# Kernel optimization log

Hardware: AMD Instinct MI355X
Metric: run time of the kernel (lower is better)

## Reference

```python
import jax, jax.numpy as jnp
import numpy as np

T, H, N = 4096, 2048, 1024  # seq_length, d_model, d_hidden
MAX_PHASE = 6.28


def setup_inputs() -> dict:
    key = jax.random.key(0)
    ks = jax.random.split(key, 9)
    inputs = jax.random.normal(ks[0], (T, H), dtype=jnp.float32)
    # LRU init (exp_param=True, r_min=0, r_max=1): lambda = exp(-exp(nu) + i*exp(theta))
    u1 = jax.random.uniform(ks[1], (N,), dtype=jnp.float32)
    u2 = jax.random.uniform(ks[2], (N,), dtype=jnp.float32)
    nu = jnp.log(-0.5 * jnp.log(u1))            # log-parameterized decay
    theta = jnp.log(MAX_PHASE * u2)             # log-parameterized phase
    # gamma_log = log(sqrt(1 - |lambda|^2)), |lambda| = exp(-exp(nu))
    gamma_log = 0.5 * jnp.log(1.0 - jnp.exp(-2.0 * jnp.exp(nu)) + 1e-8)
    B_re = jax.random.normal(ks[3], (N, H), dtype=jnp.float32) / np.sqrt(2 * H)
    B_im = jax.random.normal(ks[4], (N, H), dtype=jnp.float32) / np.sqrt(2 * H)
    C_re = jax.random.normal(ks[5], (H, N), dtype=jnp.float32) / np.sqrt(N)
    C_im = jax.random.normal(ks[6], (H, N), dtype=jnp.float32) / np.sqrt(N)
    D = jax.random.normal(ks[7], (H,), dtype=jnp.float32)
    return {"inputs": inputs, "nu": nu, "theta": theta, "gamma_log": gamma_log,
            "B_re": B_re, "B_im": B_im, "C_re": C_re, "C_im": C_im, "D": D}


def _binary_operator_diag(q_i, q_j):
    A_i, b_i = q_i
    A_j, b_j = q_j
    return (A_j * A_i, A_j * b_i + b_j)


def reference(inputs, nu, theta, gamma_log, B_re, B_im, C_re, C_im, D):
    # diag_lambda = exp(-exp(nu) + i*exp(theta))   (exp_param=True)
    diag_lambda = jnp.exp(-jnp.exp(nu) + 1j * jnp.exp(theta))      # [N] complex64
    gamma = jnp.exp(gamma_log)                                      # [N]
    B_norm = (B_re + 1j * B_im) * gamma[:, None]                    # [N, H] complex
    # Bu_t = B_norm @ u_t  ->  [T, N]
    Bu = inputs.astype(jnp.complex64) @ B_norm.T
    Lam = jnp.broadcast_to(diag_lambda[None, :], Bu.shape)          # [T, N]
    # parallel scan of diagonal linear recurrence h_t = lambda * h_{t-1} + Bu_t
    _, h = jax.lax.associative_scan(_binary_operator_diag, (Lam, Bu))
    C = C_re + 1j * C_im                                            # [H, N]
    # y_t = Re(C @ h_t) + D * u_t
    y = (h @ C.T).real + D[None, :] * inputs                        # [T, H]
    return y
```

## Files before the change

kernel.cpp:

```cpp
#include <hip/hip_runtime.h>
#include <math.h>

#define T_DIM 4096
#define H_DIM 2048
#define N_DIM 1024
#define N2    2048
#define KK    2048
#define CHUNK 64
#define NCHUNK (T_DIM / CHUNK)
#define NT    (KK / 64)

using u16    = unsigned short;
using u16x4  = __attribute__((ext_vector_type(4))) u16;
using bf16x8 = __attribute__((ext_vector_type(8))) short;
using f32x4  = __attribute__((ext_vector_type(4))) float;

typedef const __attribute__((address_space(1))) u16 glob_u16;
typedef __attribute__((address_space(3))) u16 lds_u16;

__device__ inline void gload16(const u16* g, u16* l) {
    __builtin_amdgcn_global_load_lds((glob_u16*)g, (lds_u16*)l, 16, 0, 0);
}

__device__ inline u16 f2bf(float x) {
    unsigned u = __builtin_bit_cast(unsigned, x);
    u += 0x7fffu + ((u >> 16) & 1u);
    return (u16)(u >> 16);
}
__device__ inline float bf2f(u16 x) {
    return __builtin_bit_cast(float, (unsigned)x << 16);
}

__global__ __launch_bounds__(256) void cvt_all_k(
    const float* __restrict__ U, const float* __restrict__ Bre,
    const float* __restrict__ Bim, const float* __restrict__ glog,
    const float* __restrict__ Cre, const float* __restrict__ Cim,
    u16* __restrict__ Ubf, u16* __restrict__ Bcat, u16* __restrict__ Ccat)
{
    int bid = blockIdx.x;
    if (bid < 8192) {
        size_t i = ((size_t)bid * 256 + threadIdx.x) * 4;
        float4 v = *(const float4*)(U + i);
        u16x4 o = { f2bf(v.x), f2bf(v.y), f2bf(v.z), f2bf(v.w) };
        *(u16x4*)(Ubf + i) = o;
    } else if (bid < 12288) {
        size_t i = ((size_t)(bid - 8192) * 256 + threadIdx.x) * 4;
        int n = (int)(i >> 11);
        size_t h = i & 2047;
        int nn = n & (N_DIM - 1);
        float g = expf(glog[nn]);
        const float* src = (n < N_DIM ? Bre : Bim) + (size_t)nn * H_DIM + h;
        float4 v = *(const float4*)src;
        u16x4 o = { f2bf(v.x * g), f2bf(v.y * g), f2bf(v.z * g), f2bf(v.w * g) };
        *(u16x4*)(Bcat + i) = o;
    } else {
        size_t i = ((size_t)(bid - 12288) * 256 + threadIdx.x) * 4;
        int hrow = (int)(i >> 11);
        int n = (int)(i & 2047);
        float sgn = 1.f;
        const float* src;
        if (n < N_DIM) src = Cre + (size_t)hrow * N_DIM + n;
        else { src = Cim + (size_t)hrow * N_DIM + (n - N_DIM); sgn = -1.f; }
        float4 v = *(const float4*)src;
        u16x4 o = { f2bf(v.x * sgn), f2bf(v.y * sgn), f2bf(v.z * sgn), f2bf(v.w * sgn) };
        *(u16x4*)(Ccat + i) = o;
    }
}

template <int EPI>
__global__ __launch_bounds__(512, 4) void gemm_pipe(
    const u16* __restrict__ A, const u16* __restrict__ B,
    void* __restrict__ Cout, const float* __restrict__ D,
    const u16* __restrict__ Ubf)
{
    __shared__ u16 lds[40960];

    const int tid  = threadIdx.x;
    const int wave = tid >> 6, lane = tid & 63;
    const int nbid = (blockIdx.x & 7) * 64 + (blockIdx.x >> 3);
    const int bm = nbid >> 4;
    const int bn = nbid & 15;
    const size_t row0 = (size_t)bm * 128;
    const size_t col0 = (size_t)bn * 128;
    const int kg = wave & 1;
    const int wc = (wave >> 1) & 1;
    const int wr = wave >> 2;
    const int fr = lane & 15, fq = lane >> 4;

    const int srow = wave * 16 + (lane >> 3);
    const int skc  = (lane & 7) ^ ((lane >> 3) & 7);
    const u16* aSrc = A + (row0 + srow) * KK + skc * 8;
    const u16* bSrc = B + (col0 + srow) * KK + skc * 8;
    const int stOff = wave * 1024;

    const int slot8 = ((kg * 4 + fq) ^ (fr & 7)) * 8;
    const int aOff = (wr * 64 + fr) * 64 + slot8;
    const int bOff = (wc * 64 + fr) * 64 + slot8;

    f32x4 acc[4][4] = {};

    auto STAGE_A = [&](int buf, int kt) {
        gload16(aSrc + kt * 64,            &lds[buf * 8192 + stOff]);
        gload16(aSrc + 8 * KK + kt * 64,   &lds[buf * 8192 + stOff + 512]);
    };
    auto STAGE_B = [&](int buf, int kt) {
        gload16(bSrc + kt * 64,            &lds[24576 + buf * 8192 + stOff]);
        gload16(bSrc + 8 * KK + kt * 64,   &lds[24576 + buf * 8192 + stOff + 512]);
    };

    bf16x8 fa[4], fb[4];
    auto READ_F = [&](const u16* Ab, const u16* Bb) {
#pragma unroll
        for (int m = 0; m < 4; ++m) fa[m] = *(const bf16x8*)&Ab[aOff + m * 1024];
#pragma unroll
        for (int n = 0; n < 4; ++n) fb[n] = *(const bf16x8*)&Bb[bOff + n * 1024];
    };

    STAGE_A(0, 0); STAGE_B(0, 0); STAGE_A(1, 1);
    asm volatile("s_waitcnt vmcnt(2)" ::: "memory");
    __builtin_amdgcn_s_barrier();
    READ_F(&lds[0], &lds[24576]);

    int a_cur = 0;
    for (int t = 0; t < NT; ++t) {
        if (t + 1 < NT) STAGE_B((t + 1) & 1, t + 1);
        __builtin_amdgcn_s_setprio(1);
#pragma unroll
        for (int m = 0; m < 4; ++m)
#pragma unroll
            for (int n = 0; n < 4; ++n)
                acc[m][n] = __builtin_amdgcn_mfma_f32_16x16x32_bf16(
                    fa[m], fb[n], acc[m][n], 0, 0, 0);
        __builtin_amdgcn_s_setprio(0);
        if (t + 2 < NT) {
            int a_nxt = a_cur + 2; if (a_nxt >= 3) a_nxt -= 3;
            STAGE_A(a_nxt, t + 2);
        }
        if (t + 1 < NT) {
            if (t + 2 < NT) asm volatile("s_waitcnt vmcnt(2)" ::: "memory");
            else            asm volatile("s_waitcnt vmcnt(0)" ::: "memory");
            __builtin_amdgcn_s_barrier();
            int a_n = a_cur + 1; if (a_n == 3) a_n = 0;
            READ_F(&lds[a_n * 8192], &lds[24576 + ((t + 1) & 1) * 8192]);
        }
        ++a_cur; if (a_cur == 3) a_cur = 0;
    }

    __builtin_amdgcn_s_barrier();
    const int pair = wr * 2 + wc;
    float* lf = (float*)lds;
    if (kg == 1) {
#pragma unroll
        for (int i = 0; i < 16; ++i)
            *(f32x4*)&lf[pair * 4096 + i * 256 + lane * 4] = acc[i >> 2][i & 3];
    }
    asm volatile("s_waitcnt lgkmcnt(0)" ::: "memory");
    __builtin_amdgcn_s_barrier();
    if (kg == 0) {
#pragma unroll
        for (int i = 0; i < 16; ++i) {
            f32x4 o = *(const f32x4*)&lf[pair * 4096 + i * 256 + lane * 4];
            acc[i >> 2][i & 3] += o;
        }
        const int crow = (int)row0 + wr * 64 + fq * 4;
        const int ccol = (int)col0 + wc * 64 + fr;
        float dc[4];
        if constexpr (EPI) {
#pragma unroll
            for (int n = 0; n < 4; ++n) dc[n] = D[ccol + n * 16];
        }
#pragma unroll
        for (int m = 0; m < 4; ++m)
#pragma unroll
            for (int n = 0; n < 4; ++n) {
                int cc = ccol + n * 16;
#pragma unroll
                for (int j = 0; j < 4; ++j) {
                    int r = crow + m * 16 + j;
                    size_t p = (size_t)r * N2 + cc;
                    float v = acc[m][n][j];
                    if constexpr (EPI)
                        ((float*)Cout)[p] = v + dc[n] * bf2f(Ubf[p]);
                    else
                        ((u16*)Cout)[p] = f2bf(v);
                }
            }
    }
}

__global__ __launch_bounds__(256) void carry_pass_k(const u16* __restrict__ Bu,
                                                    const float* __restrict__ nu,
                                                    const float* __restrict__ theta,
                                                    float* __restrict__ car) {
    int idx = blockIdx.x * 256 + threadIdx.x;
    int chan = idx & (N_DIM - 1);
    int chunk = idx >> 10;
    float a = expf(nu[chan]), b = expf(theta[chan]);
    float m = expf(-a), s, c;
    __sincosf(b, &s, &c);
    float lr = m * c, li = m * s;
    float hr = 0.f, hi = 0.f;
    size_t base = (size_t)chunk * CHUNK * N2 + chan;
    for (int i = 0; i < CHUNK; ++i) {
        size_t p = base + (size_t)i * N2;
        float br = bf2f(Bu[p]), bi = bf2f(Bu[p + N_DIM]);
        float nr = fmaf(lr, hr, fmaf(-li, hi, br));
        float ni = fmaf(lr, hi, fmaf(li, hr, bi));
        hr = nr; hi = ni;
    }
    car[(size_t)chunk * N2 + chan] = hr;
    car[(size_t)chunk * N2 + N_DIM + chan] = hi;
}

__global__ __launch_bounds__(256) void scan_carry_k(float* __restrict__ car,
                                                    const float* __restrict__ nu,
                                                    const float* __restrict__ theta) {
    __shared__ float sR[NCHUNK][65], sI[NCHUNK][65];
    int tid = threadIdx.x;
    int chan0 = blockIdx.x * 64;
    for (int i = tid; i < NCHUNK * 64; i += 256) {
        int ck = i >> 6, c = i & 63;
        sR[ck][c] = car[(size_t)ck * N2 + chan0 + c];
        sI[ck][c] = car[(size_t)ck * N2 + N_DIM + chan0 + c];
    }
    __syncthreads();
    if (tid < 64) {
        int chan = chan0 + tid;
        float a = expf(nu[chan]), b = expf(theta[chan]);
        float m = expf(-(float)CHUNK * a), s, c;
        __sincosf((float)CHUNK * b, &s, &c);
        float lr = m * c, li = m * s;
        float hr = sR[0][tid], hi = sI[0][tid];
        for (int ck = 1; ck < NCHUNK; ++ck) {
            float nr = fmaf(lr, hr, fmaf(-li, hi, sR[ck][tid]));
            float ni = fmaf(lr, hi, fmaf(li, hr, sI[ck][tid]));
            hr = nr; hi = ni;
            sR[ck][tid] = hr; sI[ck][tid] = hi;
        }
    }
    __syncthreads();
    for (int i = tid; i < NCHUNK * 64; i += 256) {
        int ck = i >> 6, c = i & 63;
        car[(size_t)ck * N2 + chan0 + c] = sR[ck][c];
        car[(size_t)ck * N2 + N_DIM + chan0 + c] = sI[ck][c];
    }
}

__global__ __launch_bounds__(256) void scan_out_k(const u16* __restrict__ Bu,
                                                  const float* __restrict__ car,
                                                  const float* __restrict__ nu,
                                                  const float* __restrict__ theta,
                                                  u16* __restrict__ Hbf) {
    int idx = blockIdx.x * 256 + threadIdx.x;
    int chan = idx & (N_DIM - 1);
    int chunk = idx >> 10;
    float a = expf(nu[chan]), b = expf(theta[chan]);
    float m = expf(-a), s, c;
    __sincosf(b, &s, &c);
    float lr = m * c, li = m * s;
    float hr = 0.f, hi = 0.f;
    if (chunk > 0) {
        size_t cp = (size_t)(chunk - 1) * N2 + chan;
        hr = car[cp]; hi = car[cp + N_DIM];
    }
    size_t base = (size_t)chunk * CHUNK * N2 + chan;
    for (int i = 0; i < CHUNK; ++i) {
        size_t p = base + (size_t)i * N2;
        float br = bf2f(Bu[p]), bi = bf2f(Bu[p + N_DIM]);
        float nr = fmaf(lr, hr, fmaf(-li, hi, br));
        float ni = fmaf(lr, hi, fmaf(li, hr, bi));
        hr = nr; hi = ni;
        Hbf[p] = f2bf(hr);
        Hbf[p + N_DIM] = f2bf(hi);
    }
}

extern "C" void kernel_launch(void* const* d_in, const int* in_sizes, int n_in,
                              void* d_out, int out_size, void* d_ws, size_t ws_size,
                              hipStream_t stream) {
    const float* U     = (const float*)d_in[0];
    const float* nu    = (const float*)d_in[1];
    const float* theta = (const float*)d_in[2];
    const float* glog  = (const float*)d_in[3];
    const float* Bre   = (const float*)d_in[4];
    const float* Bim   = (const float*)d_in[5];
    const float* Cre   = (const float*)d_in[6];
    const float* Cim   = (const float*)d_in[7];
    const float* Dp    = (const float*)d_in[8];
    float* Y = (float*)d_out;

    u16* Ubf  = (u16*)d_ws;
    u16* Bcat = Ubf + (size_t)T_DIM * H_DIM;
    u16* Ccat = Bcat + (size_t)N2 * H_DIM;
    u16* Hbf  = Ccat + (size_t)H_DIM * N2;
    u16* Bu   = Hbf + (size_t)T_DIM * N2;
    float* car = (float*)(Bu + (size_t)T_DIM * N2);

    cvt_all_k<<<16384, 256, 0, stream>>>(U, Bre, Bim, glog, Cre, Cim,
                                         Ubf, Bcat, Ccat);

    gemm_pipe<0><<<512, 512, 0, stream>>>(Ubf, Bcat, (void*)Bu, nullptr, nullptr);

    carry_pass_k<<<(NCHUNK * N_DIM) / 256, 256, 0, stream>>>(Bu, nu, theta, car);
    scan_carry_k<<<N_DIM / 64, 256, 0, stream>>>(car, nu, theta);
    scan_out_k<<<(NCHUNK * N_DIM) / 256, 256, 0, stream>>>(Bu, car, nu, theta, Hbf);

    gemm_pipe<1><<<512, 512, 0, stream>>>(Hbf, Ccat, (void*)Y, Dp, Ubf);
}
```

Measured before the change: 111.6 us.

## Use 256x256 split-K GEMM tiles with bf16 partials and separate combine kernel

Both GEMMs now use 256x256 output tiles and split K into two halves across blocks, in place of 128x128 tiles with an in-block K split across waves. Each half writes bf16 partial sums to its own buffer, and the scan kernels and a new combine kernel add the two partials. The goal is more operand reuse per LDS load and removal of the LDS cross-wave reduction. The cost is extra global traffic for two bf16 partial buffers, an extra elementwise launch, a plain double-buffered pipeline with full vmcnt(0) waits, and precision lost by rounding partials to bf16 before summing.

```diff
diff --git a/kernel.cpp b/kernel.cpp
--- a/kernel.cpp
+++ b/kernel.cpp
@@ -8,10 +8,11 @@
 #define KK    2048
 #define CHUNK 64
 #define NCHUNK (T_DIM / CHUNK)
-#define NT    (KK / 64)
+#define NTK   16
 
 using u16    = unsigned short;
 using u16x4  = __attribute__((ext_vector_type(4))) u16;
+using u16x8  = __attribute__((ext_vector_type(8))) u16;
 using bf16x8 = __attribute__((ext_vector_type(8))) short;
 using f32x4  = __attribute__((ext_vector_type(4))) float;
 
@@ -67,128 +68,120 @@
     }
 }
 
-template <int EPI>
-__global__ __launch_bounds__(512, 4) void gemm_pipe(
+__global__ __launch_bounds__(512, 2) void gemm_pipe(
     const u16* __restrict__ A, const u16* __restrict__ B,
-    void* __restrict__ Cout, const float* __restrict__ D,
-    const u16* __restrict__ Ubf)
+    u16* __restrict__ P0, u16* __restrict__ P1)
 {
-    __shared__ u16 lds[40960];
+    __shared__ u16 lds[65536];
 
     const int tid  = threadIdx.x;
     const int wave = tid >> 6, lane = tid & 63;
-    const int nbid = (blockIdx.x & 7) * 64 + (blockIdx.x >> 3);
-    const int bm = nbid >> 4;
-    const int bn = nbid & 15;
-    const size_t row0 = (size_t)bm * 128;
-    const size_t col0 = (size_t)bn * 128;
-    const int kg = wave & 1;
-    const int wc = (wave >> 1) & 1;
+    const int nbid = (blockIdx.x & 7) * 32 + (blockIdx.x >> 3);
+    const int ks = nbid >> 7;
+    const int rem = nbid & 127;
+    const int bm = rem >> 3;
+    const int bn = rem & 7;
+    const size_t row0 = (size_t)bm * 256;
+    const size_t col0 = (size_t)bn * 256;
+    const int ksBase = ks * 1024;
+    u16* __restrict__ Pout = ks ? P1 : P0;
+
     const int wr = wave >> 2;
+    const int wc = wave & 3;
     const int fr = lane & 15, fq = lane >> 4;
 
-    const int srow = wave * 16 + (lane >> 3);
-    const int skc  = (lane & 7) ^ ((lane >> 3) & 7);
-    const u16* aSrc = A + (row0 + srow) * KK + skc * 8;
-    const u16* bSrc = B + (col0 + srow) * KK + skc * 8;
-    const int stOff = wave * 1024;
-
-    const int slot8 = ((kg * 4 + fq) ^ (fr & 7)) * 8;
-    const int aOff = (wr * 64 + fr) * 64 + slot8;
-    const int bOff = (wc * 64 + fr) * 64 + slot8;
-
-    f32x4 acc[4][4] = {};
+    const int srow = tid >> 3;
+    const int skc  = (tid & 7) ^ (srow & 7);
+    const u16* aSrc = A + (row0 + srow) * KK + ksBase + skc * 8;
+    const u16* bSrc = B + (col0 + srow) * KK + ksBase + skc * 8;
+
+    const int slot0 = ((fq)     ^ (fr & 7)) * 8;
+    const int slot1 = ((4 + fq) ^ (fr & 7)) * 8;
+    const int aRow = (wr * 128 + fr) * 64;
+    const int bRow = (wc * 64 + fr) * 64;
+
+    f32x4 acc[8][4] = {};
 
     auto STAGE_A = [&](int buf, int kt) {
-        gload16(aSrc + kt * 64,            &lds[buf * 8192 + stOff]);
-        gload16(aSrc + 8 * KK + kt * 64,   &lds[buf * 8192 + stOff + 512]);
+#pragma unroll
+        for (int u = 0; u < 4; ++u)
+            gload16(aSrc + (size_t)(u * 64) * KK + kt * 64,
+                    &lds[buf * 16384 + u * 4096 + wave * 512]);
     };
     auto STAGE_B = [&](int buf, int kt) {
-        gload16(bSrc + kt * 64,            &lds[24576 + buf * 8192 + stOff]);
-        gload16(bSrc + 8 * KK + kt * 64,   &lds[24576 + buf * 8192 + stOff + 512]);
+#pragma unroll
+        for (int u = 0; u < 4; ++u)
+            gload16(bSrc + (size_t)(u * 64) * KK + kt * 64,
+                    &lds[32768 + buf * 16384 + u * 4096 + wave * 512]);
     };
 
-    bf16x8 fa[4], fb[4];
-    auto READ_F = [&](const u16* Ab, const u16* Bb) {
-#pragma unroll
-        for (int m = 0; m < 4; ++m) fa[m] = *(const bf16x8*)&Ab[aOff + m * 1024];
-#pragma unroll
-        for (int n = 0; n < 4; ++n) fb[n] = *(const bf16x8*)&Bb[bOff + n * 1024];
-    };
-
-    STAGE_A(0, 0); STAGE_B(0, 0); STAGE_A(1, 1);
-    asm volatile("s_waitcnt vmcnt(2)" ::: "memory");
+    STAGE_A(0, 0); STAGE_B(0, 0);
+    asm volatile("s_waitcnt vmcnt(0)" ::: "memory");
     __builtin_amdgcn_s_barrier();
-    READ_F(&lds[0], &lds[24576]);
-
-    int a_cur = 0;
-    for (int t = 0; t < NT; ++t) {
-        if (t + 1 < NT) STAGE_B((t + 1) & 1, t + 1);
-        __builtin_amdgcn_s_setprio(1);
-#pragma unroll
-        for (int m = 0; m < 4; ++m)
-#pragma unroll
-            for (int n = 0; n < 4; ++n)
-                acc[m][n] = __builtin_amdgcn_mfma_f32_16x16x32_bf16(
-                    fa[m], fb[n], acc[m][n], 0, 0, 0);
-        __builtin_amdgcn_s_setprio(0);
-        if (t + 2 < NT) {
-            int a_nxt = a_cur + 2; if (a_nxt >= 3) a_nxt -= 3;
-            STAGE_A(a_nxt, t + 2);
-        }
-        if (t + 1 < NT) {
-            if (t + 2 < NT) asm volatile("s_waitcnt vmcnt(2)" ::: "memory");
-            else            asm volatile("s_waitcnt vmcnt(0)" ::: "memory");
+
+    for (int t = 0; t < NTK; ++t) {
+        const u16* Ab = &lds[(t & 1) * 16384];
+        const u16* Bb = &lds[32768 + (t & 1) * 16384];
+
+        if (t + 1 < NTK) {
+            STAGE_A((t + 1) & 1, t + 1);
+            STAGE_B((t + 1) & 1, t + 1);
+        }
+
+        {
+            bf16x8 fb[4];
+#pragma unroll
+            for (int n = 0; n < 4; ++n) fb[n] = *(const bf16x8*)&Bb[bRow + n * 1024 + slot0];
+            __builtin_amdgcn_s_setprio(1);
+#pragma unroll
+            for (int m = 0; m < 8; ++m) {
+                bf16x8 fa = *(const bf16x8*)&Ab[aRow + m * 1024 + slot0];
+#pragma unroll
+                for (int n = 0; n < 4; ++n)
+                    acc[m][n] = __builtin_amdgcn_mfma_f32_16x16x32_bf16(
+                        fa, fb[n], acc[m][n], 0, 0, 0);
+            }
+            __builtin_amdgcn_s_setprio(0);
+        }
+        {
+            bf16x8 fb[4];
+#pragma unroll
+            for (int n = 0; n < 4; ++n) fb[n] = *(const bf16x8*)&Bb[bRow + n * 1024 + slot1];
+            __builtin_amdgcn_s_setprio(1);
+#pragma unroll
+            for (int m = 0; m < 8; ++m) {
+                bf16x8 fa = *(const bf16x8*)&Ab[aRow + m * 1024 + slot1];
+#pragma unroll
+                for (int n = 0; n < 4; ++n)
+                    acc[m][n] = __builtin_amdgcn_mfma_f32_16x16x32_bf16(
+                        fa, fb[n], acc[m][n], 0, 0, 0);
+            }
+            __builtin_amdgcn_s_setprio(0);
+        }
+
+        if (t + 1 < NTK) {
+            asm volatile("s_waitcnt vmcnt(0)" ::: "memory");
             __builtin_amdgcn_s_barrier();
-            int a_n = a_cur + 1; if (a_n == 3) a_n = 0;
-            READ_F(&lds[a_n * 8192], &lds[24576 + ((t + 1) & 1) * 8192]);
-        }
-        ++a_cur; if (a_cur == 3) a_cur = 0;
-    }
-
-    __builtin_amdgcn_s_barrier();
-    const int pair = wr * 2 + wc;
-    float* lf = (float*)lds;
-    if (kg == 1) {
-#pragma unroll
-        for (int i = 0; i < 16; ++i)
-            *(f32x4*)&lf[pair * 4096 + i * 256 + lane * 4] = acc[i >> 2][i & 3];
-    }
-    asm volatile("s_waitcnt lgkmcnt(0)" ::: "memory");
-    __builtin_amdgcn_s_barrier();
-    if (kg == 0) {
-#pragma unroll
-        for (int i = 0; i < 16; ++i) {
-            f32x4 o = *(const f32x4*)&lf[pair * 4096 + i * 256 + lane * 4];
-            acc[i >> 2][i & 3] += o;
-        }
-        const int crow = (int)row0 + wr * 64 + fq * 4;
-        const int ccol = (int)col0 + wc * 64 + fr;
-        float dc[4];
-        if constexpr (EPI) {
-#pragma unroll
-            for (int n = 0; n < 4; ++n) dc[n] = D[ccol + n * 16];
-        }
-#pragma unroll
-        for (int m = 0; m < 4; ++m)
-#pragma unroll
-            for (int n = 0; n < 4; ++n) {
-                int cc = ccol + n * 16;
-#pragma unroll
-                for (int j = 0; j < 4; ++j) {
-                    int r = crow + m * 16 + j;
-                    size_t p = (size_t)r * N2 + cc;
-                    float v = acc[m][n][j];
-                    if constexpr (EPI)
-                        ((float*)Cout)[p] = v + dc[n] * bf2f(Ubf[p]);
-                    else
-                        ((u16*)Cout)[p] = f2bf(v);
-                }
+        }
+    }
+
+    const int crow = (int)row0 + wr * 128 + fq * 4;
+    const int ccol = (int)col0 + wc * 64 + fr;
+#pragma unroll
+    for (int m = 0; m < 8; ++m)
+#pragma unroll
+        for (int n = 0; n < 4; ++n) {
+            int cc = ccol + n * 16;
+#pragma unroll
+            for (int j = 0; j < 4; ++j) {
+                int r = crow + m * 16 + j;
+                Pout[(size_t)r * N2 + cc] = f2bf(acc[m][n][j]);
             }
-    }
-}
-
-__global__ __launch_bounds__(256) void carry_pass_k(const u16* __restrict__ Bu,
+        }
+}
+
+__global__ __launch_bounds__(256) void carry_pass_k(const u16* __restrict__ P0,
+                                                    const u16* __restrict__ P1,
                                                     const float* __restrict__ nu,
                                                     const float* __restrict__ theta,
                                                     float* __restrict__ car) {
@@ -203,7 +196,8 @@
     size_t base = (size_t)chunk * CHUNK * N2 + chan;
     for (int i = 0; i < CHUNK; ++i) {
         size_t p = base + (size_t)i * N2;
-        float br = bf2f(Bu[p]), bi = bf2f(Bu[p + N_DIM]);
+        float br = bf2f(P0[p]) + bf2f(P1[p]);
+        float bi = bf2f(P0[p + N_DIM]) + bf2f(P1[p + N_DIM]);
         float nr = fmaf(lr, hr, fmaf(-li, hi, br));
         float ni = fmaf(lr, hi, fmaf(li, hr, bi));
         hr = nr; hi = ni;
@@ -246,7 +240,8 @@
     }
 }
 
-__global__ __launch_bounds__(256) void scan_out_k(const u16* __restrict__ Bu,
+__global__ __launch_bounds__(256) void scan_out_k(const u16* __restrict__ P0,
+                                                  const u16* __restrict__ P1,
                                                   const float* __restrict__ car,
                                                   const float* __restrict__ nu,
                                                   const float* __restrict__ theta,
@@ -266,13 +261,35 @@
     size_t base = (size_t)chunk * CHUNK * N2 + chan;
     for (int i = 0; i < CHUNK; ++i) {
         size_t p = base + (size_t)i * N2;
-        float br = bf2f(Bu[p]), bi = bf2f(Bu[p + N_DIM]);
+        float br = bf2f(P0[p]) + bf2f(P1[p]);
+        float bi = bf2f(P0[p + N_DIM]) + bf2f(P1[p + N_DIM]);
         float nr = fmaf(lr, hr, fmaf(-li, hi, br));
         float ni = fmaf(lr, hi, fmaf(li, hr, bi));
         hr = nr; hi = ni;
         Hbf[p] = f2bf(hr);
         Hbf[p + N_DIM] = f2bf(hi);
     }
+}
+
+__global__ __launch_bounds__(256) void combine_y_k(const u16* __restrict__ P0,
+                                                   const u16* __restrict__ P1,
+                                                   const u16* __restrict__ Ubf,
+                                                   const float* __restrict__ D,
+                                                   float* __restrict__ Y) {
+    size_t i = ((size_t)blockIdx.x * 256 + threadIdx.x) * 8;
+    u16x8 a0 = *(const u16x8*)(P0 + i);
+    u16x8 a1 = *(const u16x8*)(P1 + i);
+    u16x8 uu = *(const u16x8*)(Ubf + i);
+    int h = (int)(i & (size_t)(H_DIM - 1));
+    float4 d0 = *(const float4*)(D + h);
+    float4 d1 = *(const float4*)(D + h + 4);
+    float dv[8] = { d0.x, d0.y, d0.z, d0.w, d1.x, d1.y, d1.z, d1.w };
+    float y[8];
+#pragma unroll
+    for (int j = 0; j < 8; ++j)
+        y[j] = bf2f(a0[j]) + bf2f(a1[j]) + dv[j] * bf2f(uu[j]);
+    *(float4*)(Y + i)     = { y[0], y[1], y[2], y[3] };
+    *(float4*)(Y + i + 4) = { y[4], y[5], y[6], y[7] };
 }
 
 extern "C" void kernel_launch(void* const* d_in, const int* in_sizes, int n_in,
@@ -293,17 +310,20 @@
     u16* Bcat = Ubf + (size_t)T_DIM * H_DIM;
     u16* Ccat = Bcat + (size_t)N2 * H_DIM;
     u16* Hbf  = Ccat + (size_t)H_DIM * N2;
-    u16* Bu   = Hbf + (size_t)T_DIM * N2;
-    float* car = (float*)(Bu + (size_t)T_DIM * N2);
+    u16* P0   = Hbf + (size_t)T_DIM * N2;
+    u16* P1   = P0 + (size_t)T_DIM * N2;
+    float* car = (float*)(P1 + (size_t)T_DIM * N2);
 
     cvt_all_k<<<16384, 256, 0, stream>>>(U, Bre, Bim, glog, Cre, Cim,
                                          Ubf, Bcat, Ccat);
 
-    gemm_pipe<0><<<512, 512, 0, stream>>>(Ubf, Bcat, (void*)Bu, nullptr, nullptr);
-
-    carry_pass_k<<<(NCHUNK * N_DIM) / 256, 256, 0, stream>>>(Bu, nu, theta, car);
+    gemm_pipe<<<256, 512, 0, stream>>>(Ubf, Bcat, P0, P1);
+
+    carry_pass_k<<<(NCHUNK * N_DIM) / 256, 256, 0, stream>>>(P0, P1, nu, theta, car);
     scan_carry_k<<<N_DIM / 64, 256, 0, stream>>>(car, nu, theta);
-    scan_out_k<<<(NCHUNK * N_DIM) / 256, 256, 0, stream>>>(Bu, car, nu, theta, Hbf);
-
-    gemm_pipe<1><<<512, 512, 0, stream>>>(Hbf, Ccat, (void*)Y, Dp, Ubf);
-}
+    scan_out_k<<<(NCHUNK * N_DIM) / 256, 256, 0, stream>>>(P0, P1, car, nu, theta, Hbf);
+
+    gemm_pipe<<<256, 512, 0, stream>>>(Hbf, Ccat, P0, P1);
+
+    combine_y_k<<<(T_DIM * H_DIM / 8) / 256, 256, 0, stream>>>(P0, P1, Ubf, Dp, Y);
+}
```

New measurement: 138.4 us. 24.0% more time.

## Replace first GEMM with 256x256-tile split-K kernel writing two bf16 partials

Applied to the files above, without the earlier changes.

The first projection GEMM now uses 256x256 output tiles with K split in two across blocks, giving 256 blocks, each writing a bf16 partial sum (P0, P1). The scan kernels add the two partials when they read Bu. The goal is more data reuse per block and better MFMA density from the bigger register tile. In exchange there are extra partial writes and reads, rounding to bf16 twice, and one block per CU. The second GEMM is unchanged except for tidier wait and barrier macros.

```diff
diff --git a/kernel.cpp b/kernel.cpp
--- a/kernel.cpp
+++ b/kernel.cpp
@@ -8,10 +8,12 @@
 #define KK    2048
 #define CHUNK 64
 #define NCHUNK (T_DIM / CHUNK)
-#define NT    (KK / 64)
+#define NTK   16
+#define NT2   32
 
 using u16    = unsigned short;
 using u16x4  = __attribute__((ext_vector_type(4))) u16;
+using u16x8  = __attribute__((ext_vector_type(8))) u16;
 using bf16x8 = __attribute__((ext_vector_type(8))) short;
 using f32x4  = __attribute__((ext_vector_type(4))) float;
 
@@ -30,6 +32,12 @@
 __device__ inline float bf2f(u16 x) {
     return __builtin_bit_cast(float, (unsigned)x << 16);
 }
+
+#define WAIT_BARRIER(N) do {                                                   \
+    __builtin_amdgcn_sched_barrier(0);                                         \
+    asm volatile("s_waitcnt vmcnt(" #N ") lgkmcnt(0)\n\ts_barrier" ::: "memory"); \
+    __builtin_amdgcn_sched_barrier(0);                                         \
+} while (0)
 
 __global__ __launch_bounds__(256) void cvt_all_k(
     const float* __restrict__ U, const float* __restrict__ Bre,
@@ -67,10 +75,118 @@
     }
 }
 
-template <int EPI>
-__global__ __launch_bounds__(512, 4) void gemm_pipe(
+__global__ __launch_bounds__(512, 1) void gemm_big(
     const u16* __restrict__ A, const u16* __restrict__ B,
-    void* __restrict__ Cout, const float* __restrict__ D,
+    u16* __restrict__ P0, u16* __restrict__ P1)
+{
+    __shared__ u16 lds[65536];
+
+    const int tid  = threadIdx.x;
+    const int wave = tid >> 6, lane = tid & 63;
+    const int nbid = (blockIdx.x & 7) * 32 + (blockIdx.x >> 3);
+    const int ks = nbid >> 7;
+    const int rem = nbid & 127;
+    const int bm = rem >> 3;
+    const int bn = rem & 7;
+    const size_t row0 = (size_t)bm * 256;
+    const size_t col0 = (size_t)bn * 256;
+    u16* __restrict__ Pout = ks ? P1 : P0;
+
+    const int wr = wave >> 2;
+    const int wc = wave & 3;
+    const int fr = lane & 15, fq = lane >> 4;
+
+    const int srow = tid >> 3;
+    const int skc  = (tid & 7) ^ (srow & 7);
+    const u16* aSrc = A + (row0 + srow) * KK + ks * 1024 + skc * 8;
+    const u16* bSrc = B + (col0 + srow) * KK + ks * 1024 + skc * 8;
+
+    const int slotk[2] = { ((fq) ^ (fr & 7)) * 8, ((4 + fq) ^ (fr & 7)) * 8 };
+    const int aRow = (wr * 128 + fr) * 64;
+    const int bRow = (wc * 64 + fr) * 64;
+
+    f32x4 acc[8][4] = {};
+
+    auto STAGE = [&](int buf, int kt) {
+#pragma unroll
+        for (int u = 0; u < 4; ++u) {
+            gload16(aSrc + (size_t)(u * 64) * KK + kt * 64,
+                    &lds[buf * 16384 + u * 4096 + wave * 512]);
+            gload16(bSrc + (size_t)(u * 64) * KK + kt * 64,
+                    &lds[32768 + buf * 16384 + u * 4096 + wave * 512]);
+        }
+    };
+
+    bf16x8 fb[2][4];
+    bf16x8 faF[2][2], faG[2][2];
+
+    auto READ_FB = [&](const u16* Bb) {
+#pragma unroll
+        for (int k = 0; k < 2; ++k)
+#pragma unroll
+            for (int n = 0; n < 4; ++n)
+                fb[k][n] = *(const bf16x8*)&Bb[bRow + n * 1024 + slotk[k]];
+    };
+    auto READ_FA = [&](bf16x8 (&fa)[2][2], const u16* Ab, int q) {
+#pragma unroll
+        for (int k = 0; k < 2; ++k)
+#pragma unroll
+            for (int mm = 0; mm < 2; ++mm)
+                fa[k][mm] = *(const bf16x8*)&Ab[aRow + (q * 2 + mm) * 1024 + slotk[k]];
+    };
+    auto MFMA_Q = [&](int q, bf16x8 (&fa)[2][2]) {
+        __builtin_amdgcn_s_setprio(1);
+#pragma unroll
+        for (int k = 0; k < 2; ++k)
+#pragma unroll
+            for (int mm = 0; mm < 2; ++mm)
+#pragma unroll
+                for (int n = 0; n < 4; ++n)
+                    acc[q * 2 + mm][n] = __builtin_amdgcn_mfma_f32_16x16x32_bf16(
+                        fa[k][mm], fb[k][n], acc[q * 2 + mm][n], 0, 0, 0);
+        __builtin_amdgcn_s_setprio(0);
+    };
+
+    STAGE(0, 0);
+    WAIT_BARRIER(0);
+    READ_FB(&lds[32768]);
+    READ_FA(faF, &lds[0], 0);
+
+    for (int t = 0; t < NTK; ++t) {
+        const u16* Ab = &lds[(t & 1) * 16384];
+        const int nxt = (t & 1) ^ 1;
+        if (t + 1 < NTK) STAGE(nxt, t + 1);
+
+        READ_FA(faG, Ab, 1);  MFMA_Q(0, faF);
+        READ_FA(faF, Ab, 2);  MFMA_Q(1, faG);
+        READ_FA(faG, Ab, 3);  MFMA_Q(2, faF);
+        MFMA_Q(3, faG);
+
+        if (t + 1 < NTK) {
+            WAIT_BARRIER(0);
+            READ_FB(&lds[32768 + nxt * 16384]);
+            READ_FA(faF, &lds[nxt * 16384], 0);
+        }
+    }
+
+    const int crow = (int)row0 + wr * 128 + fq * 4;
+    const int ccol = (int)col0 + wc * 64 + fr;
+#pragma unroll
+    for (int m = 0; m < 8; ++m)
+#pragma unroll
+        for (int n = 0; n < 4; ++n) {
+            int cc = ccol + n * 16;
+#pragma unroll
+            for (int j = 0; j < 4; ++j) {
+                int r = crow + m * 16 + j;
+                Pout[(size_t)r * N2 + cc] = f2bf(acc[m][n][j]);
+            }
+        }
+}
+
+__global__ __launch_bounds__(512, 4) void gemm_kg(
+    const u16* __restrict__ A, const u16* __restrict__ B,
+    float* __restrict__ Y, const float* __restrict__ D,
     const u16* __restrict__ Ubf)
 {
     __shared__ u16 lds[40960];
@@ -100,12 +216,12 @@
     f32x4 acc[4][4] = {};
 
     auto STAGE_A = [&](int buf, int kt) {
-        gload16(aSrc + kt * 64,            &lds[buf * 8192 + stOff]);
-        gload16(aSrc + 8 * KK + kt * 64,   &lds[buf * 8192 + stOff + 512]);
+        gload16(aSrc + kt * 64,          &lds[buf * 8192 + stOff]);
+        gload16(aSrc + 8 * KK + kt * 64, &lds[buf * 8192 + stOff + 512]);
     };
     auto STAGE_B = [&](int buf, int kt) {
-        gload16(bSrc + kt * 64,            &lds[24576 + buf * 8192 + stOff]);
-        gload16(bSrc + 8 * KK + kt * 64,   &lds[24576 + buf * 8192 + stOff + 512]);
+        gload16(bSrc + kt * 64,          &lds[24576 + buf * 8192 + stOff]);
+        gload16(bSrc + 8 * KK + kt * 64, &lds[24576 + buf * 8192 + stOff + 512]);
     };
 
     bf16x8 fa[4], fb[4];
@@ -117,13 +233,12 @@
     };
 
     STAGE_A(0, 0); STAGE_B(0, 0); STAGE_A(1, 1);
-    asm volatile("s_waitcnt vmcnt(2)" ::: "memory");
-    __builtin_amdgcn_s_barrier();
+    WAIT_BARRIER(2);
     READ_F(&lds[0], &lds[24576]);
 
     int a_cur = 0;
-    for (int t = 0; t < NT; ++t) {
-        if (t + 1 < NT) STAGE_B((t + 1) & 1, t + 1);
+    for (int t = 0; t < NT2; ++t) {
+        if (t + 1 < NT2) STAGE_B((t + 1) & 1, t + 1);
         __builtin_amdgcn_s_setprio(1);
 #pragma unroll
         for (int m = 0; m < 4; ++m)
@@ -132,21 +247,20 @@
                 acc[m][n] = __builtin_amdgcn_mfma_f32_16x16x32_bf16(
                     fa[m], fb[n], acc[m][n], 0, 0, 0);
         __builtin_amdgcn_s_setprio(0);
-        if (t + 2 < NT) {
+        if (t + 2 < NT2) {
             int a_nxt = a_cur + 2; if (a_nxt >= 3) a_nxt -= 3;
             STAGE_A(a_nxt, t + 2);
         }
-        if (t + 1 < NT) {
-            if (t + 2 < NT) asm volatile("s_waitcnt vmcnt(2)" ::: "memory");
-            else            asm volatile("s_waitcnt vmcnt(0)" ::: "memory");
-            __builtin_amdgcn_s_barrier();
+        if (t + 1 < NT2) {
+            if (t + 2 < NT2) WAIT_BARRIER(2);
+            else             WAIT_BARRIER(0);
             int a_n = a_cur + 1; if (a_n == 3) a_n = 0;
             READ_F(&lds[a_n * 8192], &lds[24576 + ((t + 1) & 1) * 8192]);
         }
         ++a_cur; if (a_cur == 3) a_cur = 0;
     }
 
-    __builtin_amdgcn_s_barrier();
+    __syncthreads();
     const int pair = wr * 2 + wc;
     float* lf = (float*)lds;
     if (kg == 1) {
@@ -154,8 +268,7 @@
         for (int i = 0; i < 16; ++i)
             *(f32x4*)&lf[pair * 4096 + i * 256 + lane * 4] = acc[i >> 2][i & 3];
     }
-    asm volatile("s_waitcnt lgkmcnt(0)" ::: "memory");
-    __builtin_amdgcn_s_barrier();
+    __syncthreads();
     if (kg == 0) {
 #pragma unroll
         for (int i = 0; i < 16; ++i) {
@@ -165,10 +278,8 @@
         const int crow = (int)row0 + wr * 64 + fq * 4;
         const int ccol = (int)col0 + wc * 64 + fr;
         float dc[4];
-        if constexpr (EPI) {
-#pragma unroll
-            for (int n = 0; n < 4; ++n) dc[n] = D[ccol + n * 16];
-        }
+#pragma unroll
+        for (int n = 0; n < 4; ++n) dc[n] = D[ccol + n * 16];
 #pragma unroll
         for (int m = 0; m < 4; ++m)
 #pragma unroll
@@ -178,17 +289,14 @@
                 for (int j = 0; j < 4; ++j) {
                     int r = crow + m * 16 + j;
                     size_t p = (size_t)r * N2 + cc;
-                    float v = acc[m][n][j];
-                    if constexpr (EPI)
-                        ((float*)Cout)[p] = v + dc[n] * bf2f(Ubf[p]);
-                    else
-                        ((u16*)Cout)[p] = f2bf(v);
+                    Y[p] = acc[m][n][j] + dc[n] * bf2f(Ubf[p]);
                 }
             }
     }
 }
 
-__global__ __launch_bounds__(256) void carry_pass_k(const u16* __restrict__ Bu,
+__global__ __launch_bounds__(256) void carry_pass_k(const u16* __restrict__ P0,
+                                                    const u16* __restrict__ P1,
                                                     const float* __restrict__ nu,
                                                     const float* __restrict__ theta,
                                                     float* __restrict__ car) {
@@ -203,7 +311,8 @@
     size_t base = (size_t)chunk * CHUNK * N2 + chan;
     for (int i = 0; i < CHUNK; ++i) {
         size_t p = base + (size_t)i * N2;
-        float br = bf2f(Bu[p]), bi = bf2f(Bu[p + N_DIM]);
+        float br = bf2f(P0[p]) + bf2f(P1[p]);
+        float bi = bf2f(P0[p + N_DIM]) + bf2f(P1[p + N_DIM]);
         float nr = fmaf(lr, hr, fmaf(-li, hi, br));
         float ni = fmaf(lr, hi, fmaf(li, hr, bi));
         hr = nr; hi = ni;
@@ -246,7 +355,8 @@
     }
 }
 
-__global__ __launch_bounds__(256) void scan_out_k(const u16* __restrict__ Bu,
+__global__ __launch_bounds__(256) void scan_out_k(const u16* __restrict__ P0,
+                                                  const u16* __restrict__ P1,
                                                   const float* __restrict__ car,
                                                   const float* __restrict__ nu,
                                                   const float* __restrict__ theta,
@@ -266,7 +376,8 @@
     size_t base = (size_t)chunk * CHUNK * N2 + chan;
     for (int i = 0; i < CHUNK; ++i) {
         size_t p = base + (size_t)i * N2;
-        float br = bf2f(Bu[p]), bi = bf2f(Bu[p + N_DIM]);
+        float br = bf2f(P0[p]) + bf2f(P1[p]);
+        float bi = bf2f(P0[p + N_DIM]) + bf2f(P1[p + N_DIM]);
         float nr = fmaf(lr, hr, fmaf(-li, hi, br));
         float ni = fmaf(lr, hi, fmaf(li, hr, bi));
         hr = nr; hi = ni;
@@ -293,17 +404,18 @@
     u16* Bcat = Ubf + (size_t)T_DIM * H_DIM;
     u16* Ccat = Bcat + (size_t)N2 * H_DIM;
     u16* Hbf  = Ccat + (size_t)H_DIM * N2;
-    u16* Bu   = Hbf + (size_t)T_DIM * N2;
-    float* car = (float*)(Bu + (size_t)T_DIM * N2);
+    u16* P0   = Hbf + (size_t)T_DIM * N2;
+    u16* P1   = P0 + (size_t)T_DIM * N2;
+    float* car = (float*)(P1 + (size_t)T_DIM * N2);
 
     cvt_all_k<<<16384, 256, 0, stream>>>(U, Bre, Bim, glog, Cre, Cim,
                                          Ubf, Bcat, Ccat);
 
-    gemm_pipe<0><<<512, 512, 0, stream>>>(Ubf, Bcat, (void*)Bu, nullptr, nullptr);
-
-    carry_pass_k<<<(NCHUNK * N_DIM) / 256, 256, 0, stream>>>(Bu, nu, theta, car);
+    gemm_big<<<256, 512, 0, stream>>>(Ubf, Bcat, P0, P1);
+
+    carry_pass_k<<<(NCHUNK * N_DIM) / 256, 256, 0, stream>>>(P0, P1, nu, theta, car);
     scan_carry_k<<<N_DIM / 64, 256, 0, stream>>>(car, nu, theta);
-    scan_out_k<<<(NCHUNK * N_DIM) / 256, 256, 0, stream>>>(Bu, car, nu, theta, Hbf);
-
-    gemm_pipe<1><<<512, 512, 0, stream>>>(Hbf, Ccat, (void*)Y, Dp, Ubf);
-}
+    scan_out_k<<<(NCHUNK * N_DIM) / 256, 256, 0, stream>>>(P0, P1, car, nu, theta, Hbf);
+
+    gemm_kg<<<512, 512, 0, stream>>>(Hbf, Ccat, Y, Dp, Ubf);
+}
```

New measurement: 128.5 us. +15.2%, slower.

## Fuse per-chunk scan carry into first GEMM epilogue with interleaved complex layout

Applied to the files above, without the earlier changes.

Interleaves real and imaginary parts of the B and C projections so each 128-column GEMM tile holds 64 complete complex channels. The first GEMM now stages its bf16 output tile in LDS and runs the per-chunk local recurrence in its epilogue, writing chunk-end carries as float2. This removes the separate carry_pass kernel and its full re-read of Bu. The scan kernels use packed 32-bit loads and stores. The cost is a longer serial epilogue of 64 steps on only 128 threads per block, plus extra barriers in the GEMM.

```diff
diff --git a/kernel.cpp b/kernel.cpp
--- a/kernel.cpp
+++ b/kernel.cpp
@@ -8,7 +8,7 @@
 #define KK    2048
 #define CHUNK 64
 #define NCHUNK (T_DIM / CHUNK)
-#define NT    (KK / 64)
+#define NT2   32
 
 using u16    = unsigned short;
 using u16x4  = __attribute__((ext_vector_type(4))) u16;
@@ -30,6 +30,9 @@
 __device__ inline float bf2f(u16 x) {
     return __builtin_bit_cast(float, (unsigned)x << 16);
 }
+
+#define WAIT_BARRIER(N) \
+    asm volatile("s_waitcnt vmcnt(" #N ") lgkmcnt(0)\n\ts_barrier" ::: "memory")
 
 __global__ __launch_bounds__(256) void cvt_all_k(
     const float* __restrict__ U, const float* __restrict__ Bre,
@@ -45,24 +48,22 @@
         *(u16x4*)(Ubf + i) = o;
     } else if (bid < 12288) {
         size_t i = ((size_t)(bid - 8192) * 256 + threadIdx.x) * 4;
-        int n = (int)(i >> 11);
+        int rr = (int)(i >> 11);
         size_t h = i & 2047;
-        int nn = n & (N_DIM - 1);
-        float g = expf(glog[nn]);
-        const float* src = (n < N_DIM ? Bre : Bim) + (size_t)nn * H_DIM + h;
+        int chan = rr >> 1, part = rr & 1;
+        float g = expf(glog[chan]);
+        const float* src = (part ? Bim : Bre) + (size_t)chan * H_DIM + h;
         float4 v = *(const float4*)src;
         u16x4 o = { f2bf(v.x * g), f2bf(v.y * g), f2bf(v.z * g), f2bf(v.w * g) };
         *(u16x4*)(Bcat + i) = o;
     } else {
         size_t i = ((size_t)(bid - 12288) * 256 + threadIdx.x) * 4;
         int hrow = (int)(i >> 11);
-        int n = (int)(i & 2047);
-        float sgn = 1.f;
-        const float* src;
-        if (n < N_DIM) src = Cre + (size_t)hrow * N_DIM + n;
-        else { src = Cim + (size_t)hrow * N_DIM + (n - N_DIM); sgn = -1.f; }
-        float4 v = *(const float4*)src;
-        u16x4 o = { f2bf(v.x * sgn), f2bf(v.y * sgn), f2bf(v.z * sgn), f2bf(v.w * sgn) };
+        int n2 = (int)(i & 2047);
+        int c0 = n2 >> 1;
+        float2 re = *(const float2*)(Cre + (size_t)hrow * N_DIM + c0);
+        float2 im = *(const float2*)(Cim + (size_t)hrow * N_DIM + c0);
+        u16x4 o = { f2bf(re.x), f2bf(-im.x), f2bf(re.y), f2bf(-im.y) };
         *(u16x4*)(Ccat + i) = o;
     }
 }
@@ -71,7 +72,8 @@
 __global__ __launch_bounds__(512, 4) void gemm_pipe(
     const u16* __restrict__ A, const u16* __restrict__ B,
     void* __restrict__ Cout, const float* __restrict__ D,
-    const u16* __restrict__ Ubf)
+    const u16* __restrict__ Ubf, const float* __restrict__ nu,
+    const float* __restrict__ theta, float2* __restrict__ car2)
 {
     __shared__ u16 lds[40960];
 
@@ -100,12 +102,12 @@
     f32x4 acc[4][4] = {};
 
     auto STAGE_A = [&](int buf, int kt) {
-        gload16(aSrc + kt * 64,            &lds[buf * 8192 + stOff]);
-        gload16(aSrc + 8 * KK + kt * 64,   &lds[buf * 8192 + stOff + 512]);
+        gload16(aSrc + kt * 64,          &lds[buf * 8192 + stOff]);
+        gload16(aSrc + 8 * KK + kt * 64, &lds[buf * 8192 + stOff + 512]);
     };
     auto STAGE_B = [&](int buf, int kt) {
-        gload16(bSrc + kt * 64,            &lds[24576 + buf * 8192 + stOff]);
-        gload16(bSrc + 8 * KK + kt * 64,   &lds[24576 + buf * 8192 + stOff + 512]);
+        gload16(bSrc + kt * 64,          &lds[24576 + buf * 8192 + stOff]);
+        gload16(bSrc + 8 * KK + kt * 64, &lds[24576 + buf * 8192 + stOff + 512]);
     };
 
     bf16x8 fa[4], fb[4];
@@ -117,13 +119,12 @@
     };
 
     STAGE_A(0, 0); STAGE_B(0, 0); STAGE_A(1, 1);
-    asm volatile("s_waitcnt vmcnt(2)" ::: "memory");
-    __builtin_amdgcn_s_barrier();
+    WAIT_BARRIER(2);
     READ_F(&lds[0], &lds[24576]);
 
     int a_cur = 0;
-    for (int t = 0; t < NT; ++t) {
-        if (t + 1 < NT) STAGE_B((t + 1) & 1, t + 1);
+    for (int t = 0; t < NT2; ++t) {
+        if (t + 1 < NT2) STAGE_B((t + 1) & 1, t + 1);
         __builtin_amdgcn_s_setprio(1);
 #pragma unroll
         for (int m = 0; m < 4; ++m)
@@ -132,21 +133,20 @@
                 acc[m][n] = __builtin_amdgcn_mfma_f32_16x16x32_bf16(
                     fa[m], fb[n], acc[m][n], 0, 0, 0);
         __builtin_amdgcn_s_setprio(0);
-        if (t + 2 < NT) {
+        if (t + 2 < NT2) {
             int a_nxt = a_cur + 2; if (a_nxt >= 3) a_nxt -= 3;
             STAGE_A(a_nxt, t + 2);
         }
-        if (t + 1 < NT) {
-            if (t + 2 < NT) asm volatile("s_waitcnt vmcnt(2)" ::: "memory");
-            else            asm volatile("s_waitcnt vmcnt(0)" ::: "memory");
-            __builtin_amdgcn_s_barrier();
+        if (t + 1 < NT2) {
+            if (t + 2 < NT2) WAIT_BARRIER(2);
+            else             WAIT_BARRIER(0);
             int a_n = a_cur + 1; if (a_n == 3) a_n = 0;
             READ_F(&lds[a_n * 8192], &lds[24576 + ((t + 1) & 1) * 8192]);
         }
         ++a_cur; if (a_cur == 3) a_cur = 0;
     }
 
-    __builtin_amdgcn_s_barrier();
+    __syncthreads();
     const int pair = wr * 2 + wc;
     float* lf = (float*)lds;
     if (kg == 1) {
@@ -154,74 +154,89 @@
         for (int i = 0; i < 16; ++i)
             *(f32x4*)&lf[pair * 4096 + i * 256 + lane * 4] = acc[i >> 2][i & 3];
     }
-    asm volatile("s_waitcnt lgkmcnt(0)" ::: "memory");
-    __builtin_amdgcn_s_barrier();
+    __syncthreads();
     if (kg == 0) {
 #pragma unroll
         for (int i = 0; i < 16; ++i) {
             f32x4 o = *(const f32x4*)&lf[pair * 4096 + i * 256 + lane * 4];
             acc[i >> 2][i & 3] += o;
         }
-        const int crow = (int)row0 + wr * 64 + fq * 4;
-        const int ccol = (int)col0 + wc * 64 + fr;
-        float dc[4];
-        if constexpr (EPI) {
+    }
+    const int crow = (int)row0 + wr * 64 + fq * 4;
+    const int ccol = (int)col0 + wc * 64 + fr;
+
+    if constexpr (EPI) {
+        if (kg == 0) {
+            float dc[4];
 #pragma unroll
             for (int n = 0; n < 4; ++n) dc[n] = D[ccol + n * 16];
-        }
-#pragma unroll
-        for (int m = 0; m < 4; ++m)
-#pragma unroll
-            for (int n = 0; n < 4; ++n) {
-                int cc = ccol + n * 16;
-#pragma unroll
-                for (int j = 0; j < 4; ++j) {
-                    int r = crow + m * 16 + j;
-                    size_t p = (size_t)r * N2 + cc;
-                    float v = acc[m][n][j];
-                    if constexpr (EPI)
-                        ((float*)Cout)[p] = v + dc[n] * bf2f(Ubf[p]);
-                    else
-                        ((u16*)Cout)[p] = f2bf(v);
+#pragma unroll
+            for (int m = 0; m < 4; ++m)
+#pragma unroll
+                for (int n = 0; n < 4; ++n) {
+                    int cc = ccol + n * 16;
+#pragma unroll
+                    for (int j = 0; j < 4; ++j) {
+                        int r = crow + m * 16 + j;
+                        size_t p = (size_t)r * N2 + cc;
+                        ((float*)Cout)[p] = acc[m][n][j] + dc[n] * bf2f(Ubf[p]);
+                    }
                 }
+        }
+    } else {
+        __syncthreads();
+        u16* tile = lds;
+        if (kg == 0) {
+#pragma unroll
+            for (int m = 0; m < 4; ++m)
+#pragma unroll
+                for (int n = 0; n < 4; ++n) {
+                    int cc = ccol + n * 16;
+                    int lc = (wc * 64 + fr) + n * 16;
+#pragma unroll
+                    for (int j = 0; j < 4; ++j) {
+                        int r = crow + m * 16 + j;
+                        int lr = (wr * 64 + fq * 4 + j) + m * 16;
+                        u16 v = f2bf(acc[m][n][j]);
+                        ((u16*)Cout)[(size_t)r * N2 + cc] = v;
+                        tile[lr * 128 + lc] = v;
+                    }
+                }
+        }
+        __syncthreads();
+        if (tid < 128) {
+            int band = tid >> 6;
+            int ch   = tid & 63;
+            int chan = ((int)col0 >> 1) + ch;
+            float a = expf(nu[chan]), b = expf(theta[chan]);
+            float mm = expf(-a), s, c;
+            __sincosf(b, &s, &c);
+            float lr_ = mm * c, li_ = mm * s;
+            float hr = 0.f, hi = 0.f;
+            const u16* rowp = &tile[band * 64 * 128 + 2 * ch];
+            for (int i = 0; i < CHUNK; ++i) {
+                unsigned pr = *(const unsigned*)(rowp + i * 128);
+                float br = bf2f((u16)(pr & 0xffff));
+                float bi = bf2f((u16)(pr >> 16));
+                float nr = fmaf(lr_, hr, fmaf(-li_, hi, br));
+                float ni = fmaf(lr_, hi, fmaf(li_, hr, bi));
+                hr = nr; hi = ni;
             }
-    }
-}
-
-__global__ __launch_bounds__(256) void carry_pass_k(const u16* __restrict__ Bu,
-                                                    const float* __restrict__ nu,
-                                                    const float* __restrict__ theta,
-                                                    float* __restrict__ car) {
-    int idx = blockIdx.x * 256 + threadIdx.x;
-    int chan = idx & (N_DIM - 1);
-    int chunk = idx >> 10;
-    float a = expf(nu[chan]), b = expf(theta[chan]);
-    float m = expf(-a), s, c;
-    __sincosf(b, &s, &c);
-    float lr = m * c, li = m * s;
-    float hr = 0.f, hi = 0.f;
-    size_t base = (size_t)chunk * CHUNK * N2 + chan;
-    for (int i = 0; i < CHUNK; ++i) {
-        size_t p = base + (size_t)i * N2;
-        float br = bf2f(Bu[p]), bi = bf2f(Bu[p + N_DIM]);
-        float nr = fmaf(lr, hr, fmaf(-li, hi, br));
-        float ni = fmaf(lr, hi, fmaf(li, hr, bi));
-        hr = nr; hi = ni;
-    }
-    car[(size_t)chunk * N2 + chan] = hr;
-    car[(size_t)chunk * N2 + N_DIM + chan] = hi;
-}
-
-__global__ __launch_bounds__(256) void scan_carry_k(float* __restrict__ car,
+            int ckG = bm * 2 + band;
+            car2[(size_t)ckG * N_DIM + chan] = make_float2(hr, hi);
+        }
+    }
+}
+
+__global__ __launch_bounds__(256) void scan_carry_k(float2* __restrict__ car2,
                                                     const float* __restrict__ nu,
                                                     const float* __restrict__ theta) {
-    __shared__ float sR[NCHUNK][65], sI[NCHUNK][65];
+    __shared__ float2 sc[NCHUNK][65];
     int tid = threadIdx.x;
     int chan0 = blockIdx.x * 64;
     for (int i = tid; i < NCHUNK * 64; i += 256) {
         int ck = i >> 6, c = i & 63;
-        sR[ck][c] = car[(size_t)ck * N2 + chan0 + c];
-        sI[ck][c] = car[(size_t)ck * N2 + N_DIM + chan0 + c];
+        sc[ck][c] = car2[(size_t)ck * N_DIM + chan0 + c];
     }
     __syncthreads();
     if (tid < 64) {
@@ -230,24 +245,24 @@
         float m = expf(-(float)CHUNK * a), s, c;
         __sincosf((float)CHUNK * b, &s, &c);
         float lr = m * c, li = m * s;
-        float hr = sR[0][tid], hi = sI[0][tid];
+        float2 h = sc[0][tid];
         for (int ck = 1; ck < NCHUNK; ++ck) {
-            float nr = fmaf(lr, hr, fmaf(-li, hi, sR[ck][tid]));
-            float ni = fmaf(lr, hi, fmaf(li, hr, sI[ck][tid]));
-            hr = nr; hi = ni;
-            sR[ck][tid] = hr; sI[ck][tid] = hi;
+            float2 v = sc[ck][tid];
+            float nr = fmaf(lr, h.x, fmaf(-li, h.y, v.x));
+            float ni = fmaf(lr, h.y, fmaf(li, h.x, v.y));
+            h.x = nr; h.y = ni;
+            sc[ck][tid] = h;
         }
     }
     __syncthreads();
     for (int i = tid; i < NCHUNK * 64; i += 256) {
         int ck = i >> 6, c = i & 63;
-        car[(size_t)ck * N2 + chan0 + c] = sR[ck][c];
-        car[(size_t)ck * N2 + N_DIM + chan0 + c] = sI[ck][c];
+        car2[(size_t)ck * N_DIM + chan0 + c] = sc[ck][c];
     }
 }
 
 __global__ __launch_bounds__(256) void scan_out_k(const u16* __restrict__ Bu,
-                                                  const float* __restrict__ car,
+                                                  const float2* __restrict__ car2,
                                                   const float* __restrict__ nu,
                                                   const float* __restrict__ theta,
                                                   u16* __restrict__ Hbf) {
@@ -260,18 +275,19 @@
     float lr = m * c, li = m * s;
     float hr = 0.f, hi = 0.f;
     if (chunk > 0) {
-        size_t cp = (size_t)(chunk - 1) * N2 + chan;
-        hr = car[cp]; hi = car[cp + N_DIM];
-    }
-    size_t base = (size_t)chunk * CHUNK * N2 + chan;
+        float2 h0 = car2[(size_t)(chunk - 1) * N_DIM + chan];
+        hr = h0.x; hi = h0.y;
+    }
+    size_t base = (size_t)chunk * CHUNK * N2 + 2 * chan;
     for (int i = 0; i < CHUNK; ++i) {
         size_t p = base + (size_t)i * N2;
-        float br = bf2f(Bu[p]), bi = bf2f(Bu[p + N_DIM]);
+        unsigned pr = *(const unsigned*)(Bu + p);
+        float br = bf2f((u16)(pr & 0xffff));
+        float bi = bf2f((u16)(pr >> 16));
         float nr = fmaf(lr, hr, fmaf(-li, hi, br));
         float ni = fmaf(lr, hi, fmaf(li, hr, bi));
         hr = nr; hi = ni;
-        Hbf[p] = f2bf(hr);
-        Hbf[p + N_DIM] = f2bf(hi);
+        *(unsigned*)(Hbf + p) = (unsigned)f2bf(hr) | ((unsigned)f2bf(hi) << 16);
     }
 }
 
@@ -294,16 +310,17 @@
     u16* Ccat = Bcat + (size_t)N2 * H_DIM;
     u16* Hbf  = Ccat + (size_t)H_DIM * N2;
     u16* Bu   = Hbf + (size_t)T_DIM * N2;
-    float* car = (float*)(Bu + (size_t)T_DIM * N2);
+    float2* car2 = (float2*)(Bu + (size_t)T_DIM * N2);
 
     cvt_all_k<<<16384, 256, 0, stream>>>(U, Bre, Bim, glog, Cre, Cim,
                                          Ubf, Bcat, Ccat);
 
-    gemm_pipe<0><<<512, 512, 0, stream>>>(Ubf, Bcat, (void*)Bu, nullptr, nullptr);
-
-    carry_pass_k<<<(NCHUNK * N_DIM) / 256, 256, 0, stream>>>(Bu, nu, theta, car);
-    scan_carry_k<<<N_DIM / 64, 256, 0, stream>>>(car, nu, theta);
-    scan_out_k<<<(NCHUNK * N_DIM) / 256, 256, 0, stream>>>(Bu, car, nu, theta, Hbf);
-
-    gemm_pipe<1><<<512, 512, 0, stream>>>(Hbf, Ccat, (void*)Y, Dp, Ubf);
-}
+    gemm_pipe<0><<<512, 512, 0, stream>>>(Ubf, Bcat, (void*)Bu, nullptr,
+                                          nullptr, nu, theta, car2);
+
+    scan_carry_k<<<N_DIM / 64, 256, 0, stream>>>(car2, nu, theta);
+    scan_out_k<<<(NCHUNK * N_DIM) / 256, 256, 0, stream>>>(Bu, car2, nu, theta, Hbf);
+
+    gemm_pipe<1><<<512, 512, 0, stream>>>(Hbf, Ccat, (void*)Y, Dp,
+                                          Ubf, nullptr, nullptr, nullptr);
+}
```

Result: no change. 112.5 us (median of 2 runs) (+0.9%).
